# Kernel optimization log

Measured on AMD Instinct MI355X. Metric: run time of the kernel, lower is better.

Reference implementation:

```python
import jax, jax.numpy as jnp
import numpy as np

V, E, H, T, B, D, L = 32000, 512, 512, 128, 4, 4, 2
C0, C1 = 2000, 10000          # adaptive softmax cutoffs
NT = T - D + 1


def setup_inputs() -> dict:
    key = jax.random.key(0)
    ks = jax.random.split(key, 18)
    s = 0.02
    x = jax.random.randint(ks[0], (B, T), 1, V)
    lengths = jnp.sort(jax.random.randint(ks[1], (B,), D, T + 1))[::-1]
    lengths = lengths.at[0].set(T)
    # graph predictor output: per-layer attention matrices [B, L, T, T]
    G = jax.nn.softmax(jax.random.normal(ks[2], (B, L, T, T)), axis=-1)
    emb = (jax.random.normal(ks[3], (V, E)) * s).at[0].set(0.0)  # padding_idx=0
    enc_w_ih = jax.random.normal(ks[4], (L, 3 * H, H)) * s
    enc_w_hh = jax.random.normal(ks[5], (L, 3 * H, H)) * s
    enc_b_ih = jnp.zeros((L, 3 * H))
    enc_b_hh = jnp.zeros((L, 3 * H))
    dec_w_ih = jax.random.normal(ks[6], (3 * H, E)) * s
    dec_w_hh = jax.random.normal(ks[7], (3 * H, H)) * s
    dec_b_ih = jnp.zeros((3 * H,))
    dec_b_hh = jnp.zeros((3 * H,))
    head_w = jax.random.normal(ks[8], (C0 + 2, H)) * s
    t0_proj = jax.random.normal(ks[9], (H // 4, H)) * s
    t0_out = jax.random.normal(ks[10], (C1 - C0, H // 4)) * s
    t1_proj = jax.random.normal(ks[11], (H // 16, H)) * s
    t1_out = jax.random.normal(ks[12], (V - C1, H // 16)) * s
    return dict(x=x, lengths=lengths, G=G, emb=emb,
                enc_w_ih=enc_w_ih, enc_w_hh=enc_w_hh, enc_b_ih=enc_b_ih, enc_b_hh=enc_b_hh,
                dec_w_ih=dec_w_ih, dec_w_hh=dec_w_hh, dec_b_ih=dec_b_ih, dec_b_hh=dec_b_hh,
                head_w=head_w, t0_proj=t0_proj, t0_out=t0_out, t1_proj=t1_proj, t1_out=t1_out)


def gru_step(xt, h, w_ih, w_hh, b_ih, b_hh):
    """torch nn.GRU/GRUCell math; works on arbitrary leading dims."""
    gi = xt @ w_ih.T + b_ih
    gh = h @ w_hh.T + b_hh
    i_r, i_z, i_n = jnp.split(gi, 3, axis=-1)
    h_r, h_z, h_n = jnp.split(gh, 3, axis=-1)
    r = jax.nn.sigmoid(i_r + h_r)
    z = jax.nn.sigmoid(i_z + h_z)
    n = jnp.tanh(i_n + r * h_n)
    return (1.0 - z) * n + z * h


def adaptive_log_prob(h, head_w, t0_proj, t0_out, t1_proj, t1_out):
    """torch AdaptiveLogSoftmaxWithLoss.log_prob: h [N,H] -> [N,V]."""
    head_lp = jax.nn.log_softmax(h @ head_w.T, axis=-1)                      # [N, C0+2]
    lp0 = head_lp[:, C0:C0 + 1] + jax.nn.log_softmax((h @ t0_proj.T) @ t0_out.T, axis=-1)
    lp1 = head_lp[:, C0 + 1:C0 + 2] + jax.nn.log_softmax((h @ t1_proj.T) @ t1_out.T, axis=-1)
    return jnp.concatenate([head_lp[:, :C0], lp0, lp1], axis=-1)


def reference(x, lengths, G, emb, enc_w_ih, enc_w_hh, enc_b_ih, enc_b_hh,
              dec_w_ih, dec_w_hh, dec_b_ih, dec_b_hh,
              head_w, t0_proj, t0_out, t1_proj, t1_out):
    b = x.shape[0]
    input_f = emb[x]                      # [B,T,E] (dropout p=0)
    embedded = input_f
    # ---- encoder: graph-weighted aggregation + GRUCell per layer ----
    for l in range(enc_w_ih.shape[0]):
        wgt = jnp.einsum('bji,bjd->bid', G[:, l], input_f)   # G_l^T @ input_f
        input_f = gru_step(wgt, input_f, enc_w_ih[l], enc_w_hh[l], enc_b_ih[l], enc_b_hh[l])
    # ---- decoder: length-D GRU window per start position t ----
    t_idx = jnp.arange(NT)
    d_idx = jnp.arange(D)
    tok_idx = jnp.broadcast_to(t_idx[None, :, None] + d_idx[None, None, :] - 1, (b, NT, D))
    tok_idx = tok_idx.at[:, 0, 0].set(lengths - 1)           # t=0,d=0 uses embedded[lengths-1]
    wins = jnp.take_along_axis(embedded, tok_idx.reshape(b, -1)[:, :, None], axis=1)
    wins = wins.reshape(b, NT, D, E)
    h0 = input_f[:, :NT, :]                                  # [B,NT,H]
    def step(h, xd):
        hn = gru_step(xd, h, dec_w_ih, dec_w_hh, dec_b_ih, dec_b_hh)
        return hn, hn
    _, hs = jax.lax.scan(step, h0, jnp.moveaxis(wins, 2, 0))  # [D,B,NT,H]
    hs = jnp.moveaxis(hs, 0, 2)                               # [B,NT,D,H]
    # pad_packed_sequence zeros hidden beyond per-row lens = min(lengths - t, D)
    valid = (t_idx[None, :, None] + d_idx[None, None, :]) < lengths[:, None, None]
    hs = jnp.where(valid[..., None], hs, 0.0)
    lp = adaptive_log_prob(hs.reshape(-1, H), head_w, t0_proj, t0_out, t1_proj, t1_out)
    lp = lp.reshape(b, NT, D, V)
    # batch rows with lengths <= t were excluded and F.pad'ed with zeros
    row_valid = t_idx[None, :] < lengths[:, None]
    lp = jnp.where(row_valid[:, :, None, None], lp, 0.0)
    return lp.reshape(b, NT * D, V)
```

## Files before the change

### kernel.cpp

```cpp
#include <hip/hip_runtime.h>
#include <hip/hip_bf16.h>

typedef __hip_bfloat16 bf16;
typedef __attribute__((ext_vector_type(8))) short short8v;
typedef __attribute__((ext_vector_type(4))) float float4v;

#define V_    32000
#define E_    512
#define H_    512
#define T_    128
#define B_    4
#define D_    4
#define L_    2
#define C0_   2000
#define C1_   10000
#define NT_   125
#define NROW_ 2000
#define NH_   2002
#define NTOTC 2162
#define NSLOT 252

__device__ __forceinline__ float bf2f(bf16 v) { return __bfloat162float(v); }
__device__ __forceinline__ unsigned short f2bfu(float f) {
    bf16 h = __float2bfloat16(f);
    union { bf16 h; unsigned short u; } cv; cv.h = h; return cv.u;
}
__device__ __forceinline__ float ld1(const void* p, size_t i, int bf) {
    return bf ? bf2f(((const bf16*)p)[i]) : ((const float*)p)[i];
}
__device__ __forceinline__ void st1(void* p, size_t i, int bf, float v) {
    if (bf) ((unsigned short*)p)[i] = f2bfu(v);
    else    ((float*)p)[i] = v;
}

__device__ __forceinline__ void lse_push(float z, float& m, float& s) {
    if (z <= m) { s += __expf(z - m); }
    else        { s = s * __expf(m - z) + 1.0f; m = z; }
}
__device__ __forceinline__ void lse_merge(float m2, float s2, float& m, float& s) {
    float mm = fmaxf(m, m2);
    s = s * __expf(m - mm) + s2 * __expf(m2 - mm);
    m = mm;
}

__global__ void k_detect(const void* __restrict__ G, int* __restrict__ flag) {
    int t = threadIdx.x;
    float s32 = 0.0f;
    for (int k = t; k < 128; k += 64) s32 += ((const float*)G)[k];
    for (int off = 32; off; off >>= 1) s32 += __shfl_down(s32, off);
    if (t == 0) {
        float e32 = fabsf(s32 - 1.0f);
        *flag = (e32 < 0.05f) ? 0 : 1;
    }
}

struct ConvArgs {
    const void* src[9];
    unsigned int off[10];
};
__global__ void k_wconv(ConvArgs a, unsigned short* __restrict__ wb,
                        const int* __restrict__ flagp) {
    const int bf = *flagp;
    unsigned int total = a.off[9];
    for (unsigned int i = blockIdx.x * 256 + threadIdx.x; i < total;
         i += gridDim.x * 256) {
        int seg = 0;
        while (i >= a.off[seg + 1]) seg++;
        wb[i] = f2bfu(ld1(a.src[seg], i - a.off[seg], bf));
    }
}

__global__ void k_embed(const int* __restrict__ x, const void* __restrict__ emb,
                        float* __restrict__ embedded, float* __restrict__ f0,
                        unsigned short* __restrict__ f0b,
                        const int* __restrict__ flagp) {
    const int bf = *flagp;
    int i = blockIdx.x * 256 + threadIdx.x;
    int bt = i >> 9, e = i & 511;
    int tok = x[bt];
    float v = ld1(emb, (size_t)tok * E_ + e, bf);
    embedded[i] = v; f0[i] = v; f0b[i] = f2bfu(v);
}

__global__ void k_wgt(const void* __restrict__ G, const float* __restrict__ f,
                      unsigned short* __restrict__ wgtb, int l,
                      const int* __restrict__ flagp) {
    const int bf = *flagp;
    int i = blockIdx.x * 256 + threadIdx.x;
    int e = i & 511;
    int bi = i >> 9;
    int b = bi >> 7, ip = bi & 127;
    size_t gbase = ((size_t)(b * L_ + l) * T_ * T_) + ip;
    const float* fb = f + (size_t)b * T_ * E_ + e;
    float acc = 0.0f;
    #pragma unroll 4
    for (int j = 0; j < T_; ++j)
        acc = fmaf(ld1(G, gbase + (size_t)j * T_, bf), fb[(size_t)j * E_], acc);
    wgtb[i] = f2bfu(acc);
}

struct GemmP {
    const unsigned short* A0;
    const unsigned short* A1;
    const unsigned short* W;
    unsigned long long w1off;
    int M, N, K, Nlse;
    float* Zg; int ldz; int zcol1;
    const void* bias0; const void* bias1; int boff;
    void* out; int outColOff;
    float* stats;
    unsigned short* p0b;
    unsigned short* p1b;
    float* lsep; int slotBase;
    const float* corr;
    const int* lengths;
    const int* flagp;
};

template<int MODE>
__global__ void k_gemm(GemmP p) {
    const int bf = *p.flagp;
    const int zsel = blockIdx.z;
    const unsigned short* A  = zsel ? p.A1 : p.A0;
    const unsigned short* Bw = p.W + (zsel ? p.w1off : 0ull);
    const int M = p.M, N = p.N, K = p.K;
    const int bx = blockIdx.x, by = blockIdx.y;
    const int m0 = by * 128, n0 = bx * 128;
    const int t = threadIdx.x;
    const int wave = t >> 6, lane = t & 63;
    const int wm = wave >> 1, wn = wave & 1;
    const int quad = lane >> 4, l16 = lane & 15;

    __shared__ __align__(16) unsigned short As[128 * 40];
    __shared__ __align__(16) unsigned short Bs[128 * 40];
    __shared__ float pm[128][2], ps[128][2];

    float4v acc[4][4];
    #pragma unroll
    for (int mi = 0; mi < 4; ++mi)
        #pragma unroll
        for (int ni = 0; ni < 4; ++ni)
            acc[mi][ni] = (float4v){0.f, 0.f, 0.f, 0.f};

    for (int k0 = 0; k0 < K; k0 += 32) {
        if (k0) __syncthreads();
        #pragma unroll
        for (int i = 0; i < 2; ++i) {
            int idx = t + i * 256;
            int row = idx >> 2, seg = idx & 3;
            uint4 av = {0u, 0u, 0u, 0u};
            int gm = m0 + row;
            if (gm < M) av = *(const uint4*)(A + (size_t)gm * K + k0 + seg * 8);
            *(uint4*)(&As[row * 40 + seg * 8]) = av;
            uint4 bv = {0u, 0u, 0u, 0u};
            int gn = n0 + row;
            if (gn < N) bv = *(const uint4*)(Bw + (size_t)gn * K + k0 + seg * 8);
            *(uint4*)(&Bs[row * 40 + seg * 8]) = bv;
        }
        __syncthreads();
        short8v af[4], bfv[4];
        #pragma unroll
        for (int mi = 0; mi < 4; ++mi)
            af[mi] = *(const short8v*)(As + (wm * 64 + mi * 16 + l16) * 40 + quad * 8);
        #pragma unroll
        for (int ni = 0; ni < 4; ++ni)
            bfv[ni] = *(const short8v*)(Bs + (wn * 64 + ni * 16 + l16) * 40 + quad * 8);
        #pragma unroll
        for (int mi = 0; mi < 4; ++mi)
            #pragma unroll
            for (int ni = 0; ni < 4; ++ni)
                acc[mi][ni] = __builtin_amdgcn_mfma_f32_16x16x32_bf16(
                    af[mi], bfv[ni], acc[mi][ni], 0, 0, 0);
    }

    if (MODE == 0) {
        const void* bias = zsel ? p.bias1 : p.bias0;
        const int zcol = zsel ? p.zcol1 : 0;
        #pragma unroll
        for (int mi = 0; mi < 4; ++mi)
            #pragma unroll
            for (int r = 0; r < 4; ++r) {
                int grow = m0 + wm * 64 + mi * 16 + quad * 4 + r;
                if (grow >= M) continue;
                #pragma unroll
                for (int ni = 0; ni < 4; ++ni) {
                    int gcol = n0 + wn * 64 + ni * 16 + l16;
                    if (gcol < N)
                        p.Zg[(size_t)grow * p.ldz + zcol + gcol] =
                            acc[mi][ni][r] + ld1(bias, p.boff + gcol, bf);
                }
            }
    } else if (MODE == 1) {
        #pragma unroll
        for (int mi = 0; mi < 4; ++mi)
            #pragma unroll
            for (int r = 0; r < 4; ++r) {
                int grow = m0 + wm * 64 + mi * 16 + quad * 4 + r;
                if (grow >= M) continue;
                #pragma unroll
                for (int ni = 0; ni < 4; ++ni) {
                    int gcol = n0 + wn * 64 + ni * 16 + l16;
                    float v = acc[mi][ni][r];
                    if (gcol >= C0_ && gcol < NH_) p.stats[grow * 8 + 2 + (gcol - C0_)] = v;
                    else if (gcol >= NH_ && gcol < 2130) p.p0b[grow * 128 + (gcol - NH_)] = f2bfu(v);
                    else if (gcol >= 2130 && gcol < NTOTC) p.p1b[grow * 32 + (gcol - 2130)] = f2bfu(v);
                }
            }
    } else if (MODE >= 3) {
        const int crIdx = MODE - 3;
        #pragma unroll
        for (int mi = 0; mi < 4; ++mi)
            #pragma unroll
            for (int r = 0; r < 4; ++r) {
                int grow = m0 + wm * 64 + mi * 16 + quad * 4 + r;
                if (grow >= M) continue;
                int b = grow / 500;
                int tt = (grow - b * 500) >> 2;
                bool valid = tt < p.lengths[b];
                float cr = p.corr[grow * 4 + crIdx];
                #pragma unroll
                for (int ni = 0; ni < 4; ++ni) {
                    int gcol = n0 + wn * 64 + ni * 16 + l16;
                    if (gcol < N) {
                        float v = valid ? (acc[mi][ni][r] - cr) : 0.0f;
                        st1(p.out, (size_t)grow * V_ + p.outColOff + gcol, bf, v);
                    }
                }
            }
    }

    if (MODE == 1 || MODE == 2) {
        const int Nlse = p.Nlse;
        #pragma unroll
        for (int mi = 0; mi < 4; ++mi) {
            #pragma unroll
            for (int r = 0; r < 4; ++r) {
                float m = -1e30f, s = 0.0f;
                #pragma unroll
                for (int ni = 0; ni < 4; ++ni) {
                    int gcol = n0 + wn * 64 + ni * 16 + l16;
                    if (gcol < Nlse) lse_push(acc[mi][ni][r], m, s);
                }
                #pragma unroll
                for (int off = 1; off < 16; off <<= 1) {
                    float m2 = __shfl_xor(m, off), s2 = __shfl_xor(s, off);
                    lse_merge(m2, s2, m, s);
                }
                if (l16 == 0) {
                    int rl = wm * 64 + mi * 16 + quad * 4 + r;
                    pm[rl][wn] = m; ps[rl][wn] = s;
                }
            }
        }
        __syncthreads();
        if (t < 128) {
            int grow = m0 + t;
            if (grow < M) {
                float m = pm[t][0], s = ps[t][0];
                lse_merge(pm[t][1], ps[t][1], m, s);
                float* dst = p.lsep + ((size_t)grow * NSLOT + p.slotBase + bx) * 2;
                dst[0] = m; dst[1] = s;
            }
        }
    }
}

__device__ __forceinline__ float gru2(float i_r, float i_z, float i_n,
                                      float h_r, float h_z, float h_n, float h) {
    float r = 1.0f / (1.0f + __expf(-(i_r + h_r)));
    float z = 1.0f / (1.0f + __expf(-(i_z + h_z)));
    float n = tanhf(i_n + r * h_n);
    return (1.0f - z) * n + z * h;
}

__global__ void k_apply_enc(const float* __restrict__ gates,
                            const float* __restrict__ hprev,
                            float* __restrict__ hnext,
                            unsigned short* __restrict__ hnextb) {
    int i = blockIdx.x * 256 + threadIdx.x;
    int row = i >> 9, k = i & 511;
    const float* g = gates + (size_t)row * 3072;
    float v = gru2(g[k], g[512 + k], g[1024 + k],
                   g[1536 + k], g[2048 + k], g[2560 + k], hprev[i]);
    hnext[i] = v; hnextb[i] = f2bfu(v);
}

__global__ void k_h0(const float* __restrict__ ffin, float* __restrict__ hdec,
                     unsigned short* __restrict__ hdecb) {
    int i = blockIdx.x * 256 + threadIdx.x;
    int row = i >> 9, e = i & 511;
    int b = row / NT_, t = row - b * NT_;
    float v = ffin[((size_t)(b * T_ + t) << 9) + e];
    hdec[i] = v; hdecb[i] = f2bfu(v);
}

__global__ void k_winall(const float* __restrict__ embedded,
                         const int* __restrict__ lengths,
                         unsigned short* __restrict__ winb) {
    int i = blockIdx.x * 256 + threadIdx.x;
    int e = i & 511;
    int wr = i >> 9;
    int d = wr / 500, row = wr - d * 500;
    int b = row / NT_, t = row - b * NT_;
    int tok = (d == 0 && t == 0) ? (lengths[b] - 1) : (t + d - 1);
    winb[i] = f2bfu(embedded[((size_t)(b * T_ + tok) << 9) + e]);
}

__global__ void k_apply_dec(const float* __restrict__ gih,
                            const float* __restrict__ ghh,
                            float* __restrict__ hdec,
                            unsigned short* __restrict__ hdecb,
                            unsigned short* __restrict__ hsb,
                            const int* __restrict__ lengths, int d) {
    int i = blockIdx.x * 256 + threadIdx.x;
    int row = i >> 9, k = i & 511;
    int b = row / NT_, t = row - b * NT_;
    const float* gi = gih + (size_t)(d * 500 + row) * 1536;
    const float* gh = ghh + (size_t)row * 1536;
    float hn = gru2(gi[k], gi[512 + k], gi[1024 + k],
                    gh[k], gh[512 + k], gh[1024 + k], hdec[i]);
    hdec[i] = hn; hdecb[i] = f2bfu(hn);
    bool valid = (t + d) < lengths[b];
    hsb[(((size_t)row * D_ + d) << 9) + k] = valid ? f2bfu(hn) : (unsigned short)0;
}

__global__ void k_corr2(const float* __restrict__ lsep, const float* __restrict__ stats,
                        float* __restrict__ corr) {
    int r = blockIdx.x * 256 + threadIdx.x;
    if (r >= NROW_) return;
    const float* P = lsep + (size_t)r * NSLOT * 2;
    float m = -1e30f, s = 0.0f;
    for (int i = 0; i < 17; ++i)  lse_merge(P[2 * i], P[2 * i + 1], m, s);
    float ch = m + logf(s);
    float lp0 = stats[r * 8 + 2] - ch;
    float lp1 = stats[r * 8 + 3] - ch;
    m = -1e30f; s = 0.0f;
    for (int i = 17; i < 80; ++i) lse_merge(P[2 * i], P[2 * i + 1], m, s);
    float ct0 = m + logf(s);
    m = -1e30f; s = 0.0f;
    for (int i = 80; i < 252; ++i) lse_merge(P[2 * i], P[2 * i + 1], m, s);
    float ct1 = m + logf(s);
    corr[r * 4 + 0] = ch;
    corr[r * 4 + 1] = ct0 - lp0;
    corr[r * 4 + 2] = ct1 - lp1;
}

#define OFF_EMB    0u
#define OFF_FA     262144u
#define OFF_FB     524288u
#define OFF_FAB    786432u
#define OFF_FBB    917504u
#define OFF_WGTB   1048576u
#define OFF_GATES  1179648u
#define OFF_GIH    2752512u
#define OFF_GHH    5824512u
#define OFF_HDEC   6592512u
#define OFF_HDECB  6848512u
#define OFF_WINB   6976512u
#define OFF_HSB    7488512u
#define OFF_P0B    8000512u
#define OFF_P1B    8128512u
#define OFF_STATS  8160512u
#define OFF_CORR   8176512u
#define OFF_LSEP   8184512u
#define OFF_WB     9192512u
#define OFF_FLAG   12969264u

#define WO_ENCIH   0u
#define WO_ENCHH   1572864u
#define WO_DECIH   3145728u
#define WO_DECHH   3932160u
#define WO_W1      4718592u
#define WO_T0O     5825536u
#define WO_T1O     6849536u
#define WO_END     7553504u

static inline GemmP mkp(const unsigned short* A0, const unsigned short* A1,
                        const unsigned short* W, unsigned long long w1off,
                        int M, int N, int K, int Nlse,
                        float* Zg, int ldz, int zcol1,
                        const void* bias0, const void* bias1, int boff,
                        void* out, int outColOff, float* stats,
                        unsigned short* p0b, unsigned short* p1b,
                        float* lsep, int slotBase, const float* corr,
                        const int* lengths, const int* flagp) {
    GemmP p;
    p.A0 = A0; p.A1 = A1; p.W = W; p.w1off = w1off;
    p.M = M; p.N = N; p.K = K; p.Nlse = Nlse;
    p.Zg = Zg; p.ldz = ldz; p.zcol1 = zcol1;
    p.bias0 = bias0; p.bias1 = bias1; p.boff = boff;
    p.out = out; p.outColOff = outColOff; p.stats = stats;
    p.p0b = p0b; p.p1b = p1b; p.lsep = lsep; p.slotBase = slotBase;
    p.corr = corr; p.lengths = lengths; p.flagp = flagp;
    return p;
}

extern "C" void kernel_launch(void* const* d_in, const int* in_sizes, int n_in,
                              void* d_out, int out_size, void* d_ws, size_t ws_size,
                              hipStream_t stream) {
    (void)in_sizes; (void)n_in; (void)out_size; (void)ws_size;
    const int*  x        = (const int*)d_in[0];
    const int*  lengths  = (const int*)d_in[1];
    const void* G        = d_in[2];
    const void* emb      = d_in[3];
    const void* enc_w_ih = d_in[4];
    const void* enc_w_hh = d_in[5];
    const void* enc_b_ih = d_in[6];
    const void* enc_b_hh = d_in[7];
    const void* dec_w_ih = d_in[8];
    const void* dec_w_hh = d_in[9];
    const void* dec_b_ih = d_in[10];
    const void* dec_b_hh = d_in[11];
    const void* head_w   = d_in[12];
    const void* t0_proj  = d_in[13];
    const void* t0_out   = d_in[14];
    const void* t1_proj  = d_in[15];
    const void* t1_out   = d_in[16];

    float* ws = (float*)d_ws;
    float* embedded = ws + OFF_EMB;
    float* fA    = ws + OFF_FA;
    float* fB    = ws + OFF_FB;
    unsigned short* fAb  = (unsigned short*)(ws + OFF_FAB);
    unsigned short* fBb  = (unsigned short*)(ws + OFF_FBB);
    unsigned short* wgtb = (unsigned short*)(ws + OFF_WGTB);
    float* gates = ws + OFF_GATES;
    float* gih   = ws + OFF_GIH;
    float* ghh   = ws + OFF_GHH;
    float* hdec  = ws + OFF_HDEC;
    unsigned short* hdecb = (unsigned short*)(ws + OFF_HDECB);
    unsigned short* winb  = (unsigned short*)(ws + OFF_WINB);
    unsigned short* hsb   = (unsigned short*)(ws + OFF_HSB);
    unsigned short* p0b   = (unsigned short*)(ws + OFF_P0B);
    unsigned short* p1b   = (unsigned short*)(ws + OFF_P1B);
    float* stats = ws + OFF_STATS;
    float* corr  = ws + OFF_CORR;
    float* lsep  = ws + OFF_LSEP;
    unsigned short* WB = (unsigned short*)(ws + OFF_WB);
    int* flagp = (int*)(ws + OFF_FLAG);
    void* out = d_out;

    k_detect<<<1, 64, 0, stream>>>(G, flagp);

    ConvArgs ca;
    ca.src[0] = enc_w_ih; ca.src[1] = enc_w_hh; ca.src[2] = dec_w_ih;
    ca.src[3] = dec_w_hh; ca.src[4] = head_w;   ca.src[5] = t0_proj;
    ca.src[6] = t1_proj;  ca.src[7] = t0_out;   ca.src[8] = t1_out;
    ca.off[0] = WO_ENCIH; ca.off[1] = WO_ENCHH; ca.off[2] = WO_DECIH;
    ca.off[3] = WO_DECHH; ca.off[4] = WO_W1;
    ca.off[5] = WO_W1 + 2002u * 512u;
    ca.off[6] = WO_W1 + 2130u * 512u;
    ca.off[7] = WO_T0O;   ca.off[8] = WO_T1O;   ca.off[9] = WO_END;
    k_wconv<<<4096, 256, 0, stream>>>(ca, WB, flagp);

    k_embed<<<1024, 256, 0, stream>>>(x, emb, embedded, fA, fAb, flagp);

    k_wgt<<<1024, 256, 0, stream>>>(G, fA, wgtb, 0, flagp);
    k_gemm<0><<<dim3(12, 4, 2), 256, 0, stream>>>(mkp(
        wgtb, fAb, WB + WO_ENCIH, (unsigned long long)(WO_ENCHH - WO_ENCIH),
        512, 1536, 512, 0, gates, 3072, 1536, enc_b_ih, enc_b_hh, 0,
        nullptr, 0, nullptr, nullptr, nullptr, nullptr, 0, nullptr, lengths, flagp));
    k_apply_enc<<<1024, 256, 0, stream>>>(gates, fA, fB, fBb);

    k_wgt<<<1024, 256, 0, stream>>>(G, fB, wgtb, 1, flagp);
    k_gemm<0><<<dim3(12, 4, 2), 256, 0, stream>>>(mkp(
        wgtb, fBb, WB + WO_ENCIH + 786432u, (unsigned long long)(WO_ENCHH - WO_ENCIH),
        512, 1536, 512, 0, gates, 3072, 1536, enc_b_ih, enc_b_hh, 1536,
        nullptr, 0, nullptr, nullptr, nullptr, nullptr, 0, nullptr, lengths, flagp));
    k_apply_enc<<<1024, 256, 0, stream>>>(gates, fB, fA, fAb);

    k_h0<<<1000, 256, 0, stream>>>(fA, hdec, hdecb);
    k_winall<<<4000, 256, 0, stream>>>(embedded, lengths, winb);
    k_gemm<0><<<dim3(12, 16, 1), 256, 0, stream>>>(mkp(
        winb, nullptr, WB + WO_DECIH, 0ull, 2000, 1536, 512, 0,
        gih, 1536, 0, dec_b_ih, nullptr, 0,
        nullptr, 0, nullptr, nullptr, nullptr, nullptr, 0, nullptr, lengths, flagp));
    for (int d = 0; d < D_; ++d) {
        k_gemm<0><<<dim3(12, 4, 1), 256, 0, stream>>>(mkp(
            hdecb, nullptr, WB + WO_DECHH, 0ull, 500, 1536, 512, 0,
            ghh, 1536, 0, dec_b_hh, nullptr, 0,
            nullptr, 0, nullptr, nullptr, nullptr, nullptr, 0, nullptr, lengths, flagp));
        k_apply_dec<<<1000, 256, 0, stream>>>(gih, ghh, hdec, hdecb, hsb, lengths, d);
    }

    k_gemm<1><<<dim3(17, 16, 1), 256, 0, stream>>>(mkp(
        hsb, nullptr, WB + WO_W1, 0ull, NROW_, NTOTC, 512, NH_,
        nullptr, 0, 0, nullptr, nullptr, 0, nullptr, 0,
        stats, p0b, p1b, lsep, 0, nullptr, lengths, flagp));
    k_gemm<2><<<dim3(63, 16, 1), 256, 0, stream>>>(mkp(
        p0b, nullptr, WB + WO_T0O, 0ull, NROW_, 8000, 128, 8000,
        nullptr, 0, 0, nullptr, nullptr, 0, nullptr, 0,
        stats, nullptr, nullptr, lsep, 17, nullptr, lengths, flagp));
    k_gemm<2><<<dim3(172, 16, 1), 256, 0, stream>>>(mkp(
        p1b, nullptr, WB + WO_T1O, 0ull, NROW_, 22000, 32, 22000,
        nullptr, 0, 0, nullptr, nullptr, 0, nullptr, 0,
        stats, nullptr, nullptr, lsep, 80, nullptr, lengths, flagp));

    k_corr2<<<8, 256, 0, stream>>>(lsep, stats, corr);

    k_gemm<3><<<dim3(16, 16, 1), 256, 0, stream>>>(mkp(
        hsb, nullptr, WB + WO_W1, 0ull, NROW_, C0_, 512, 0,
        nullptr, 0, 0, nullptr, nullptr, 0, out, 0,
        nullptr, nullptr, nullptr, nullptr, 0, corr, lengths, flagp));
    k_gemm<4><<<dim3(63, 16, 1), 256, 0, stream>>>(mkp(
        p0b, nullptr, WB + WO_T0O, 0ull, NROW_, 8000, 128, 0,
        nullptr, 0, 0, nullptr, nullptr, 0, out, C0_,
        nullptr, nullptr, nullptr, nullptr, 0, corr, lengths, flagp));
    k_gemm<5><<<dim3(172, 16, 1), 256, 0, stream>>>(mkp(
        p1b, nullptr, WB + WO_T1O, 0ull, NROW_, 22000, 32, 0,
        nullptr, 0, 0, nullptr, nullptr, 0, out, C1_,
        nullptr, nullptr, nullptr, nullptr, 0, corr, lengths, flagp));
}
```

Before: 801.5 us.

## Store raw logits in first pass and apply log-softmax correction in one fix kernel

The output GEMMs now write raw logits straight into the output buffer during the LSE-statistics pass, in fp16 when the output is bf16. A single vectorized fix-up kernel then subtracts the per-row correction and applies the validity mask, so the second round of three recompute GEMMs is gone. Several small prep kernels are merged (weight conversion with embedding, h0 with window gather) and launch bounds are added to the GEMM. The cost is an extra read-modify-write pass over the large output, and staging through fp16 then converting to bf16 may lose precision or overflow for large values.

```diff
diff --git a/kernel.cpp b/kernel.cpp
--- a/kernel.cpp
+++ b/kernel.cpp
@@ -1,5 +1,6 @@
 #include <hip/hip_runtime.h>
 #include <hip/hip_bf16.h>
+#include <hip/hip_fp16.h>
 
 typedef __hip_bfloat16 bf16;
 typedef __attribute__((ext_vector_type(8))) short short8v;
@@ -28,10 +29,6 @@
 __device__ __forceinline__ float ld1(const void* p, size_t i, int bf) {
     return bf ? bf2f(((const bf16*)p)[i]) : ((const float*)p)[i];
 }
-__device__ __forceinline__ void st1(void* p, size_t i, int bf, float v) {
-    if (bf) ((unsigned short*)p)[i] = f2bfu(v);
-    else    ((float*)p)[i] = v;
-}
 
 __device__ __forceinline__ void lse_push(float z, float& m, float& s) {
     if (z <= m) { s += __expf(z - m); }
@@ -58,28 +55,28 @@
     const void* src[9];
     unsigned int off[10];
 };
-__global__ void k_wconv(ConvArgs a, unsigned short* __restrict__ wb,
-                        const int* __restrict__ flagp) {
+__global__ void k_wembed(ConvArgs a, unsigned short* __restrict__ wb,
+                         const int* __restrict__ flagp,
+                         const int* __restrict__ x, const void* __restrict__ emb,
+                         float* __restrict__ embedded, float* __restrict__ f0,
+                         unsigned short* __restrict__ f0b) {
     const int bf = *flagp;
-    unsigned int total = a.off[9];
-    for (unsigned int i = blockIdx.x * 256 + threadIdx.x; i < total;
-         i += gridDim.x * 256) {
-        int seg = 0;
-        while (i >= a.off[seg + 1]) seg++;
-        wb[i] = f2bfu(ld1(a.src[seg], i - a.off[seg], bf));
-    }
-}
-
-__global__ void k_embed(const int* __restrict__ x, const void* __restrict__ emb,
-                        float* __restrict__ embedded, float* __restrict__ f0,
-                        unsigned short* __restrict__ f0b,
-                        const int* __restrict__ flagp) {
-    const int bf = *flagp;
-    int i = blockIdx.x * 256 + threadIdx.x;
-    int bt = i >> 9, e = i & 511;
-    int tok = x[bt];
-    float v = ld1(emb, (size_t)tok * E_ + e, bf);
-    embedded[i] = v; f0[i] = v; f0b[i] = f2bfu(v);
+    if (blockIdx.x < 1024) {
+        int i = blockIdx.x * 256 + threadIdx.x;
+        int bt = i >> 9, e = i & 511;
+        int tok = x[bt];
+        float v = ld1(emb, (size_t)tok * E_ + e, bf);
+        embedded[i] = v; f0[i] = v; f0b[i] = f2bfu(v);
+    } else {
+        unsigned int total = a.off[9];
+        unsigned int stride = (gridDim.x - 1024) * 256;
+        for (unsigned int i = (blockIdx.x - 1024) * 256 + threadIdx.x; i < total;
+             i += stride) {
+            int seg = 0;
+            while (i >= a.off[seg + 1]) seg++;
+            wb[i] = f2bfu(ld1(a.src[seg], i - a.off[seg], bf));
+        }
+    }
 }
 
 __global__ void k_wgt(const void* __restrict__ G, const float* __restrict__ f,
@@ -107,20 +104,24 @@
     int M, N, K, Nlse;
     float* Zg; int ldz; int zcol1;
     const void* bias0; const void* bias1; int boff;
-    void* out; int outColOff;
+    void* zraw; int outColOff;
     float* stats;
     unsigned short* p0b;
     unsigned short* p1b;
     float* lsep; int slotBase;
-    const float* corr;
     const int* lengths;
     const int* flagp;
 };
 
+__device__ __forceinline__ void zstore(void* zraw, size_t i, int bf, float v) {
+    if (bf) ((__half*)zraw)[i] = __float2half(v);
+    else    ((float*)zraw)[i]  = v;
+}
+
 template<int MODE>
-__global__ void k_gemm(GemmP p) {
+__global__ __launch_bounds__(256, 2) void k_gemm(GemmP p) {
     const int bf = *p.flagp;
-    const int zsel = blockIdx.z;
+    const int zsel = (MODE == 0) ? blockIdx.z : 0;
     const unsigned short* A  = zsel ? p.A1 : p.A0;
     const unsigned short* Bw = p.W + (zsel ? p.w1off : 0ull);
     const int M = p.M, N = p.N, K = p.K;
@@ -201,30 +202,25 @@
                 for (int ni = 0; ni < 4; ++ni) {
                     int gcol = n0 + wn * 64 + ni * 16 + l16;
                     float v = acc[mi][ni][r];
-                    if (gcol >= C0_ && gcol < NH_) p.stats[grow * 8 + 2 + (gcol - C0_)] = v;
-                    else if (gcol >= NH_ && gcol < 2130) p.p0b[grow * 128 + (gcol - NH_)] = f2bfu(v);
-                    else if (gcol >= 2130 && gcol < NTOTC) p.p1b[grow * 32 + (gcol - 2130)] = f2bfu(v);
+                    if (gcol < C0_) zstore(p.zraw, (size_t)grow * V_ + gcol, bf, v);
+                    else if (gcol < NH_) p.stats[grow * 8 + 2 + (gcol - C0_)] = v;
+                    else if (gcol < 2130) p.p0b[grow * 128 + (gcol - NH_)] = f2bfu(v);
+                    else if (gcol < NTOTC) p.p1b[grow * 32 + (gcol - 2130)] = f2bfu(v);
                 }
             }
-    } else if (MODE >= 3) {
-        const int crIdx = MODE - 3;
+    } else {
         #pragma unroll
         for (int mi = 0; mi < 4; ++mi)
             #pragma unroll
             for (int r = 0; r < 4; ++r) {
                 int grow = m0 + wm * 64 + mi * 16 + quad * 4 + r;
                 if (grow >= M) continue;
-                int b = grow / 500;
-                int tt = (grow - b * 500) >> 2;
-                bool valid = tt < p.lengths[b];
-                float cr = p.corr[grow * 4 + crIdx];
                 #pragma unroll
                 for (int ni = 0; ni < 4; ++ni) {
                     int gcol = n0 + wn * 64 + ni * 16 + l16;
-                    if (gcol < N) {
-                        float v = valid ? (acc[mi][ni][r] - cr) : 0.0f;
-                        st1(p.out, (size_t)grow * V_ + p.outColOff + gcol, bf, v);
-                    }
+                    if (gcol < N)
+                        zstore(p.zraw, (size_t)grow * V_ + p.outColOff + gcol, bf,
+                               acc[mi][ni][r]);
                 }
             }
     }
@@ -285,25 +281,27 @@
     hnext[i] = v; hnextb[i] = f2bfu(v);
 }
 
-__global__ void k_h0(const float* __restrict__ ffin, float* __restrict__ hdec,
-                     unsigned short* __restrict__ hdecb) {
+__global__ void k_h0win(const float* __restrict__ embedded,
+                        const float* __restrict__ ffin,
+                        const int* __restrict__ lengths,
+                        unsigned short* __restrict__ winb,
+                        float* __restrict__ hdec,
+                        unsigned short* __restrict__ hdecb) {
     int i = blockIdx.x * 256 + threadIdx.x;
-    int row = i >> 9, e = i & 511;
-    int b = row / NT_, t = row - b * NT_;
-    float v = ffin[((size_t)(b * T_ + t) << 9) + e];
-    hdec[i] = v; hdecb[i] = f2bfu(v);
-}
-
-__global__ void k_winall(const float* __restrict__ embedded,
-                         const int* __restrict__ lengths,
-                         unsigned short* __restrict__ winb) {
-    int i = blockIdx.x * 256 + threadIdx.x;
-    int e = i & 511;
-    int wr = i >> 9;
-    int d = wr / 500, row = wr - d * 500;
-    int b = row / NT_, t = row - b * NT_;
-    int tok = (d == 0 && t == 0) ? (lengths[b] - 1) : (t + d - 1);
-    winb[i] = f2bfu(embedded[((size_t)(b * T_ + tok) << 9) + e]);
+    if (i < 1024000) {
+        int e = i & 511;
+        int wr = i >> 9;
+        int d = wr / 500, row = wr - d * 500;
+        int b = row / NT_, t = row - b * NT_;
+        int tok = (d == 0 && t == 0) ? (lengths[b] - 1) : (t + d - 1);
+        winb[i] = f2bfu(embedded[((size_t)(b * T_ + tok) << 9) + e]);
+    } else {
+        int j = i - 1024000;
+        int row = j >> 9, e = j & 511;
+        int b = row / NT_, t = row - b * NT_;
+        float v = ffin[((size_t)(b * T_ + t) << 9) + e];
+        hdec[j] = v; hdecb[j] = f2bfu(v);
+    }
 }
 
 __global__ void k_apply_dec(const float* __restrict__ gih,
@@ -343,6 +341,40 @@
     corr[r * 4 + 0] = ch;
     corr[r * 4 + 1] = ct0 - lp0;
     corr[r * 4 + 2] = ct1 - lp1;
+}
+
+__global__ void k_fix(const float* __restrict__ corr,
+                      const int* __restrict__ lengths, void* __restrict__ out,
+                      const int* __restrict__ flagp) {
+    const int bf = *flagp;
+    int idx = blockIdx.x * 256 + threadIdx.x;
+    if (idx >= NROW_ * (V_ / 8)) return;
+    int row = idx / (V_ / 8);
+    int col = (idx - row * (V_ / 8)) * 8;
+    int b = row / 500;
+    int tt = (row - b * 500) >> 2;
+    bool valid = tt < lengths[b];
+    int cri = (col < C0_) ? 0 : (col < C1_ ? 1 : 2);
+    float cr = corr[row * 4 + cri];
+    size_t base = (size_t)row * V_ + col;
+    if (bf) {
+        unsigned short* p16 = (unsigned short*)out + base;
+        union { uint4 u; __half h[8]; } in;
+        in.u = *(const uint4*)p16;
+        union { uint4 u; unsigned short s[8]; } o;
+        #pragma unroll
+        for (int j = 0; j < 8; ++j)
+            o.s[j] = f2bfu(valid ? (__half2float(in.h[j]) - cr) : 0.0f);
+        *(uint4*)p16 = o.u;
+    } else {
+        float* op = (float*)out + base;
+        float4 a = *(float4*)op, c = *(float4*)(op + 4);
+        float4 ra = valid ? (float4){a.x - cr, a.y - cr, a.z - cr, a.w - cr}
+                          : (float4){0.f, 0.f, 0.f, 0.f};
+        float4 rc = valid ? (float4){c.x - cr, c.y - cr, c.z - cr, c.w - cr}
+                          : (float4){0.f, 0.f, 0.f, 0.f};
+        *(float4*)op = ra; *(float4*)(op + 4) = rc;
+    }
 }
 
 #define OFF_EMB    0u
@@ -380,18 +412,18 @@
                         int M, int N, int K, int Nlse,
                         float* Zg, int ldz, int zcol1,
                         const void* bias0, const void* bias1, int boff,
-                        void* out, int outColOff, float* stats,
+                        void* zraw, int outColOff, float* stats,
                         unsigned short* p0b, unsigned short* p1b,
-                        float* lsep, int slotBase, const float* corr,
+                        float* lsep, int slotBase,
                         const int* lengths, const int* flagp) {
     GemmP p;
     p.A0 = A0; p.A1 = A1; p.W = W; p.w1off = w1off;
     p.M = M; p.N = N; p.K = K; p.Nlse = Nlse;
     p.Zg = Zg; p.ldz = ldz; p.zcol1 = zcol1;
     p.bias0 = bias0; p.bias1 = bias1; p.boff = boff;
-    p.out = out; p.outColOff = outColOff; p.stats = stats;
+    p.zraw = zraw; p.outColOff = outColOff; p.stats = stats;
     p.p0b = p0b; p.p1b = p1b; p.lsep = lsep; p.slotBase = slotBase;
-    p.corr = corr; p.lengths = lengths; p.flagp = flagp;
+    p.lengths = lengths; p.flagp = flagp;
     return p;
 }
 
@@ -451,63 +483,51 @@
     ca.off[5] = WO_W1 + 2002u * 512u;
     ca.off[6] = WO_W1 + 2130u * 512u;
     ca.off[7] = WO_T0O;   ca.off[8] = WO_T1O;   ca.off[9] = WO_END;
-    k_wconv<<<4096, 256, 0, stream>>>(ca, WB, flagp);
-
-    k_embed<<<1024, 256, 0, stream>>>(x, emb, embedded, fA, fAb, flagp);
+    k_wembed<<<3072, 256, 0, stream>>>(ca, WB, flagp, x, emb, embedded, fA, fAb);
 
     k_wgt<<<1024, 256, 0, stream>>>(G, fA, wgtb, 0, flagp);
     k_gemm<0><<<dim3(12, 4, 2), 256, 0, stream>>>(mkp(
         wgtb, fAb, WB + WO_ENCIH, (unsigned long long)(WO_ENCHH - WO_ENCIH),
         512, 1536, 512, 0, gates, 3072, 1536, enc_b_ih, enc_b_hh, 0,
-        nullptr, 0, nullptr, nullptr, nullptr, nullptr, 0, nullptr, lengths, flagp));
+        nullptr, 0, nullptr, nullptr, nullptr, nullptr, 0, lengths, flagp));
     k_apply_enc<<<1024, 256, 0, stream>>>(gates, fA, fB, fBb);
 
     k_wgt<<<1024, 256, 0, stream>>>(G, fB, wgtb, 1, flagp);
     k_gemm<0><<<dim3(12, 4, 2), 256, 0, stream>>>(mkp(
         wgtb, fBb, WB + WO_ENCIH + 786432u, (unsigned long long)(WO_ENCHH - WO_ENCIH),
         512, 1536, 512, 0, gates, 3072, 1536, enc_b_ih, enc_b_hh, 1536,
-        nullptr, 0, nullptr, nullptr, nullptr, nullptr, 0, nullptr, lengths, flagp));
+        nullptr, 0, nullptr, nullptr, nullptr, nullptr, 0, lengths, flagp));
     k_apply_enc<<<1024, 256, 0, stream>>>(gates, fB, fA, fAb);
 
-    k_h0<<<1000, 256, 0, stream>>>(fA, hdec, hdecb);
-    k_winall<<<4000, 256, 0, stream>>>(embedded, lengths, winb);
+    k_h0win<<<5000, 256, 0, stream>>>(embedded, fA, lengths, winb, hdec, hdecb);
+
     k_gemm<0><<<dim3(12, 16, 1), 256, 0, stream>>>(mkp(
         winb, nullptr, WB + WO_DECIH, 0ull, 2000, 1536, 512, 0,
         gih, 1536, 0, dec_b_ih, nullptr, 0,
-        nullptr, 0, nullptr, nullptr, nullptr, nullptr, 0, nullptr, lengths, flagp));
+        nullptr, 0, nullptr, nullptr, nullptr, nullptr, 0, lengths, flagp));
+
     for (int d = 0; d < D_; ++d) {
         k_gemm<0><<<dim3(12, 4, 1), 256, 0, stream>>>(mkp(
             hdecb, nullptr, WB + WO_DECHH, 0ull, 500, 1536, 512, 0,
             ghh, 1536, 0, dec_b_hh, nullptr, 0,
-            nullptr, 0, nullptr, nullptr, nullptr, nullptr, 0, nullptr, lengths, flagp));
+            nullptr, 0, nullptr, nullptr, nullptr, nullptr, 0, lengths, flagp));
         k_apply_dec<<<1000, 256, 0, stream>>>(gih, ghh, hdec, hdecb, hsb, lengths, d);
     }
 
     k_gemm<1><<<dim3(17, 16, 1), 256, 0, stream>>>(mkp(
         hsb, nullptr, WB + WO_W1, 0ull, NROW_, NTOTC, 512, NH_,
-        nullptr, 0, 0, nullptr, nullptr, 0, nullptr, 0,
-        stats, p0b, p1b, lsep, 0, nullptr, lengths, flagp));
+        nullptr, 0, 0, nullptr, nullptr, 0, out, 0,
+        stats, p0b, p1b, lsep, 0, lengths, flagp));
     k_gemm<2><<<dim3(63, 16, 1), 256, 0, stream>>>(mkp(
         p0b, nullptr, WB + WO_T0O, 0ull, NROW_, 8000, 128, 8000,
-        nullptr, 0, 0, nullptr, nullptr, 0, nullptr, 0,
-        stats, nullptr, nullptr, lsep, 17, nullptr, lengths, flagp));
+        nullptr, 0, 0, nullptr, nullptr, 0, out, C0_,
+        stats, nullptr, nullptr, lsep, 17, lengths, flagp));
     k_gemm<2><<<dim3(172, 16, 1), 256, 0, stream>>>(mkp(
         p1b, nullptr, WB + WO_T1O, 0ull, NROW_, 22000, 32, 22000,
-        nullptr, 0, 0, nullptr, nullptr, 0, nullptr, 0,
-        stats, nullptr, nullptr, lsep, 80, nullptr, lengths, flagp));
+        nullptr, 0, 0, nullptr, nullptr, 0, out, C1_,
+        stats, nullptr, nullptr, lsep, 80, lengths, flagp));
 
     k_corr2<<<8, 256, 0, stream>>>(lsep, stats, corr);
 
-    k_gemm<3><<<dim3(16, 16, 1), 256, 0, stream>>>(mkp(
-        hsb, nullptr, WB + WO_W1, 0ull, NROW_, C0_, 512, 0,
-        nullptr, 0, 0, nullptr, nullptr, 0, out, 0,
-        nullptr, nullptr, nullptr, nullptr, 0, corr, lengths, flagp));
-    k_gemm<4><<<dim3(63, 16, 1), 256, 0, stream>>>(mkp(
-        p0b, nullptr, WB + WO_T0O, 0ull, NROW_, 8000, 128, 0,
-        nullptr, 0, 0, nullptr, nullptr, 0, out, C0_,
-        nullptr, nullptr, nullptr, nullptr, 0, corr, lengths, flagp));
-    k_gemm<5><<<dim3(172, 16, 1), 256, 0, stream>>>(mkp(
-        p1b, nullptr, WB + WO_T1O, 0ull, NROW_, 22000, 32, 0,
-        nullptr, 0, 0, nullptr, nullptr, 0, out, C1_,
-        nullptr, nullptr, nullptr, nullptr, 0, corr, lengths, flagp));
-}
+    k_fix<<<31250, 256, 0, stream>>>(corr, lengths, out, flagp);
+}
```

Result: faster. 783.9 us (-2.2%).
